# Optimization experiments

Hardware: AMD Instinct MI355X
Metric: run time of the kernel (lower is better)

## Reference

```python
import jax, jax.numpy as jnp
import numpy as np

B, N, C, L, E = 8, 8192, 256, 4, 131072  # graphs, nodes/graph, channels (in=hidden=out), layers, edges/graph


def setup_inputs() -> dict:
    key = jax.random.key(0)
    ks = jax.random.split(key, 9)
    batch_node_tsr = jax.random.normal(ks[0], (B, N, C), jnp.float32)
    edge_index = jax.random.randint(ks[1], (B, 2, E), 0, N, jnp.int32)
    batch_last_node_idx_list = jnp.arange(1, B + 1, dtype=jnp.int32) * N - 1
    s1 = 1.0 / np.sqrt(C)
    s2 = 1.0 / np.sqrt(2 * C)
    # Base GraphConv layers: out = x @ Wr.T + sum_nbr(x) @ Wn.T + b  (all CxC since in=hidden=out)
    base_Wr = jax.random.uniform(ks[2], (L, C, C), jnp.float32, -s1, s1)
    base_Wn = jax.random.uniform(ks[3], (L, C, C), jnp.float32, -s1, s1)
    base_b = jax.random.uniform(ks[4], (L, C), jnp.float32, -s1, s1)
    # Adapter GraphConv layers take concatenated (2C) input
    adapt_Wr = jax.random.uniform(ks[5], (L, C, 2 * C), jnp.float32, -s2, s2)
    adapt_Wn = jax.random.uniform(ks[6], (L, C, 2 * C), jnp.float32, -s2, s2)
    adapt_b = jax.random.uniform(ks[7], (L, C), jnp.float32, -s2, s2)
    return dict(batch_node_tsr=batch_node_tsr, base_Wr=base_Wr, base_Wn=base_Wn,
                base_b=base_b, adapt_Wr=adapt_Wr, adapt_Wn=adapt_Wn, adapt_b=adapt_b,
                edge_index=edge_index, batch_last_node_idx_list=batch_last_node_idx_list)


def reference(batch_node_tsr, base_Wr, base_Wn, base_b, adapt_Wr, adapt_Wn, adapt_b,
              edge_index, batch_last_node_idx_list):
    # Batch graphs PyG-style: offset per-graph node indices into one big graph
    offsets = (jnp.arange(B, dtype=edge_index.dtype) * N)[:, None]  # [B,1]
    src = (edge_index[:, 0, :] + offsets).reshape(-1)  # [B*E]
    dst = (edge_index[:, 1, :] + offsets).reshape(-1)  # [B*E]
    x = batch_node_tsr.reshape(B * N, C)

    def gconv(h, Wr, Wn, b):
        # GraphConv: root transform + sum-aggregated neighbor transform
        agg = jax.ops.segment_sum(h[src], dst, num_segments=B * N)
        return h @ Wr.T + agg @ Wn.T + b

    # Base encoder pass, keeping all latent embeds
    lat = [x]
    for i in range(L):
        lat.append(jax.nn.relu(gconv(lat[-1], base_Wr[i], base_Wn[i], base_b[i])))
    base_batch_embed = lat[-1].reshape(B, N, C)

    # Adapter pass: concat(base_latent[i+1], curr) -> adapter GraphConv -> relu
    curr = x
    for i in range(L):
        curr = jax.nn.relu(gconv(jnp.concatenate([lat[i + 1], curr], axis=-1),
                                 adapt_Wr[i], adapt_Wn[i], adapt_b[i]))
    adapter_batch_embed = curr.reshape(B, N, C)
    return base_batch_embed, adapter_batch_embed
```

## Files before the change

### kernel.cpp

```cpp
#include <hip/hip_runtime.h>

#define B_ 8
#define N_ 8192
#define C_ 256
#define L_ 4
#define E_ 131072
#define BN_ 65536
#define EDGES_ 1048576

typedef __attribute__((ext_vector_type(8))) short short8;
typedef __attribute__((ext_vector_type(4))) float f32x4;

__device__ __forceinline__ unsigned short f2bf(float f){
  unsigned int u = __builtin_bit_cast(unsigned int, f);
  u += 0x7fffu + ((u >> 16) & 1u);
  return (unsigned short)(u >> 16);
}
__device__ __forceinline__ float bf2f(unsigned short h){
  unsigned int u = ((unsigned int)h) << 16;
  return __builtin_bit_cast(float, u);
}

__launch_bounds__(256)
__global__ void cvt_bf16_k(const float* __restrict__ in, unsigned short* __restrict__ out, int n4){
  int t = blockIdx.x * 256 + threadIdx.x;
  if (t >= n4) return;
  float4 v = ((const float4*)in)[t];
  ushort4 o;
  o.x = f2bf(v.x); o.y = f2bf(v.y); o.z = f2bf(v.z); o.w = f2bf(v.w);
  ((ushort4*)out)[t] = o;
}

__launch_bounds__(256)
__global__ void hist_k(const int* __restrict__ ei, int* __restrict__ cnt){
  int t = blockIdx.x * 256 + threadIdx.x;
  int b = t >> 17, e = t & (E_ - 1);
  int dst = ei[b * (2 * E_) + E_ + e];
  atomicAdd(&cnt[(b << 13) + dst], 1);
}

__launch_bounds__(256)
__global__ void scan_k(const int* __restrict__ cnt, int* __restrict__ row_ptr, int* __restrict__ cursor){
  __shared__ int lsum[256];
  int t = threadIdx.x;
  int base = t << 8;
  int s = 0;
  for (int i = 0; i < 256; ++i) s += cnt[base + i];
  lsum[t] = s;
  __syncthreads();
  for (int d = 1; d < 256; d <<= 1){
    int v = (t >= d) ? lsum[t - d] : 0;
    __syncthreads();
    lsum[t] += v;
    __syncthreads();
  }
  int off = lsum[t] - s;
  for (int i = 0; i < 256; ++i){
    row_ptr[base + i] = off;
    cursor[base + i]  = off;
    off += cnt[base + i];
  }
  if (t == 255) row_ptr[BN_] = off;
}

__launch_bounds__(256)
__global__ void scat_k(const int* __restrict__ ei, int* __restrict__ cursor, int* __restrict__ col){
  int t = blockIdx.x * 256 + threadIdx.x;
  int b = t >> 17, e = t & (E_ - 1);
  int src = ei[b * (2 * E_) + e];
  int dst = ei[b * (2 * E_) + E_ + e];
  int pos = atomicAdd(&cursor[(b << 13) + dst], 1);
  col[pos] = (b << 13) + src;
}

__launch_bounds__(256)
__global__ void agg_k(const unsigned short* __restrict__ feat, const int* __restrict__ row_ptr,
                      const int* __restrict__ col, unsigned short* __restrict__ out){
  int w = threadIdx.x >> 6, lane = threadIdx.x & 63;
  int g = blockIdx.x & 7, sblk = blockIdx.x >> 3;
  int node = (g << 13) + (sblk << 2) + w;
  int beg = row_ptr[node], end = row_ptr[node + 1];
  int ch = lane << 2;
  float a0=0,a1=0,a2=0,a3=0,b0=0,b1=0,b2=0,b3=0;
  int e = beg;
  for (; e + 2 <= end; e += 2){
    int s0 = col[e], s1 = col[e + 1];
    ushort4 v0 = *(const ushort4*)(feat + ((size_t)s0 << 8) + ch);
    ushort4 v1 = *(const ushort4*)(feat + ((size_t)s1 << 8) + ch);
    a0 += bf2f(v0.x); a1 += bf2f(v0.y); a2 += bf2f(v0.z); a3 += bf2f(v0.w);
    b0 += bf2f(v1.x); b1 += bf2f(v1.y); b2 += bf2f(v1.z); b3 += bf2f(v1.w);
  }
  if (e < end){
    int s0 = col[e];
    ushort4 v0 = *(const ushort4*)(feat + ((size_t)s0 << 8) + ch);
    a0 += bf2f(v0.x); a1 += bf2f(v0.y); a2 += bf2f(v0.z); a3 += bf2f(v0.w);
  }
  ushort4 o;
  o.x = f2bf(a0 + b0); o.y = f2bf(a1 + b1); o.z = f2bf(a2 + b2); o.w = f2bf(a3 + b3);
  *(ushort4*)(out + ((size_t)node << 8) + ch) = o;
}

#define GLDS16(gp, lp) __builtin_amdgcn_global_load_lds( \
    (const __attribute__((address_space(1))) void*)(gp), \
    (__attribute__((address_space(3))) void*)(lp), 16, 0, 0)

template<int P>
__launch_bounds__(256)
__global__ void gemm_k(const unsigned short* __restrict__ A0, const unsigned short* __restrict__ A1,
                       const unsigned short* __restrict__ A2, const unsigned short* __restrict__ A3,
                       const unsigned short* __restrict__ W0, const unsigned short* __restrict__ W1,
                       const unsigned short* __restrict__ W2, const unsigned short* __restrict__ W3,
                       int ldw, const float* __restrict__ bias,
                       unsigned short* __restrict__ outb, float* __restrict__ outf){
  __shared__ unsigned short a_t[128 * 32];
  __shared__ unsigned short b_t[128 * 32];
  const unsigned short* As[4] = {A0, A1, A2, A3};
  const unsigned short* Ws[4] = {W0, W1, W2, W3};
  const int tn = blockIdx.x & 1, tm = blockIdx.x >> 1;
  const int m0 = tm << 7, n0 = tn << 7;
  const int t = threadIdx.x, lane = t & 63;
  const int w = t >> 6, wr = w >> 1, wc = w & 1;
  const int lrow = lane & 15, kg = lane >> 4;
  f32x4 acc[4][4] = {};
#pragma unroll
  for (int p = 0; p < P; ++p){
    const unsigned short* A = As[p] + (size_t)m0 * C_;
    const unsigned short* W = Ws[p] + (size_t)n0 * ldw;
    for (int k0 = 0; k0 < C_; k0 += 32){
#pragma unroll
      for (int c = t; c < 512; c += 256){
        int row = c >> 2, seg = c & 3;
        GLDS16(A + row * C_  + k0 + seg * 8, &a_t[c * 8]);
        GLDS16(W + row * ldw + k0 + seg * 8, &b_t[c * 8]);
      }
      __syncthreads();
      short8 af[4], bfr[4];
#pragma unroll
      for (int m = 0; m < 4; ++m)
        af[m] = *(const short8*)&a_t[((wr << 6) + (m << 4) + lrow) * 32 + (kg << 3)];
#pragma unroll
      for (int n = 0; n < 4; ++n)
        bfr[n] = *(const short8*)&b_t[((wc << 6) + (n << 4) + lrow) * 32 + (kg << 3)];
#pragma unroll
      for (int m = 0; m < 4; ++m)
#pragma unroll
        for (int n = 0; n < 4; ++n)
          acc[m][n] = __builtin_amdgcn_mfma_f32_16x16x32_bf16(af[m], bfr[n], acc[m][n], 0, 0, 0);
      __syncthreads();
    }
  }
#pragma unroll
  for (int n = 0; n < 4; ++n){
    int colg = n0 + (wc << 6) + (n << 4) + lrow;
    float bv = bias[colg];
#pragma unroll
    for (int m = 0; m < 4; ++m){
      int rbase = m0 + (wr << 6) + (m << 4) + (kg << 2);
#pragma unroll
      for (int j = 0; j < 4; ++j){
        float v = acc[m][n][j] + bv;
        v = v > 0.f ? v : 0.f;
        size_t idx = (size_t)(rbase + j) * C_ + colg;
        outb[idx] = f2bf(v);
        if (outf) outf[idx] = v;
      }
    }
  }
}

extern "C" void kernel_launch(void* const* d_in, const int* in_sizes, int n_in,
                              void* d_out, int out_size, void* d_ws, size_t ws_size,
                              hipStream_t stream){
  const float* x_f   = (const float*)d_in[0];
  const float* bWr_f = (const float*)d_in[1];
  const float* bWn_f = (const float*)d_in[2];
  const float* bB    = (const float*)d_in[3];
  const float* aWr_f = (const float*)d_in[4];
  const float* aWn_f = (const float*)d_in[5];
  const float* aB    = (const float*)d_in[6];
  const int*   ei    = (const int*)d_in[7];
  float* out = (float*)d_out;
  (void)in_sizes; (void)n_in; (void)out_size; (void)ws_size;

  char* p = (char*)d_ws;
  const size_t BUF = (size_t)BN_ * C_ * sizeof(unsigned short);
  auto alloc = [&](size_t bytes){ void* r = (void*)p; p += (bytes + 255) & ~(size_t)255; return r; };
  unsigned short* xb   = (unsigned short*)alloc(BUF);
  unsigned short* latA = (unsigned short*)alloc(BUF);
  unsigned short* latB = (unsigned short*)alloc(BUF);
  unsigned short* curA = (unsigned short*)alloc(BUF);
  unsigned short* curB = (unsigned short*)alloc(BUF);
  unsigned short* agg0 = (unsigned short*)alloc(BUF);
  unsigned short* agg1 = (unsigned short*)alloc(BUF);
  unsigned short* wbR  = (unsigned short*)alloc((size_t)L_ * C_ * C_ * 2);
  unsigned short* wbN  = (unsigned short*)alloc((size_t)L_ * C_ * C_ * 2);
  unsigned short* waR  = (unsigned short*)alloc((size_t)L_ * C_ * 2 * C_ * 2);
  unsigned short* waN  = (unsigned short*)alloc((size_t)L_ * C_ * 2 * C_ * 2);
  int* cnt     = (int*)alloc((size_t)BN_ * 4);
  int* row_ptr = (int*)alloc((size_t)(BN_ + 1) * 4);
  int* cursor  = (int*)alloc((size_t)BN_ * 4);
  int* colx    = (int*)alloc((size_t)EDGES_ * 4);

  cvt_bf16_k<<<BN_ * C_ / 4 / 256, 256, 0, stream>>>(x_f, xb, BN_ * C_ / 4);
  cvt_bf16_k<<<L_ * C_ * C_ / 4 / 256, 256, 0, stream>>>(bWr_f, wbR, L_ * C_ * C_ / 4);
  cvt_bf16_k<<<L_ * C_ * C_ / 4 / 256, 256, 0, stream>>>(bWn_f, wbN, L_ * C_ * C_ / 4);
  cvt_bf16_k<<<L_ * C_ * 2 * C_ / 4 / 256, 256, 0, stream>>>(aWr_f, waR, L_ * C_ * 2 * C_ / 4);
  cvt_bf16_k<<<L_ * C_ * 2 * C_ / 4 / 256, 256, 0, stream>>>(aWn_f, waN, L_ * C_ * 2 * C_ / 4);

  hipMemsetAsync(cnt, 0, (size_t)BN_ * 4, stream);
  hist_k<<<EDGES_ / 256, 256, 0, stream>>>(ei, cnt);
  scan_k<<<1, 256, 0, stream>>>(cnt, row_ptr, cursor);
  scat_k<<<EDGES_ / 256, 256, 0, stream>>>(ei, cursor, colx);

  const int AGG_GRID  = BN_ / 4;
  const int GEMM_GRID = (BN_ / 128) * (C_ / 128);

  const size_t WB = (size_t)C_ * C_;
  const size_t WA = (size_t)C_ * 2 * C_;

  agg_k<<<AGG_GRID, 256, 0, stream>>>(xb, row_ptr, colx, agg0);
  gemm_k<2><<<GEMM_GRID, 256, 0, stream>>>(xb, agg0, nullptr, nullptr,
      wbR, wbN, nullptr, nullptr, C_, bB, latA, nullptr);
  agg_k<<<AGG_GRID, 256, 0, stream>>>(latA, row_ptr, colx, agg1);
  gemm_k<2><<<GEMM_GRID, 256, 0, stream>>>(latA, agg1, nullptr, nullptr,
      wbR + WB, wbN + WB, nullptr, nullptr, C_, bB + 256, latB, nullptr);
  gemm_k<4><<<GEMM_GRID, 256, 0, stream>>>(latA, xb, agg1, agg0,
      waR, waR + 256, waN, waN + 256, 2 * C_, aB, curA, nullptr);
  agg_k<<<AGG_GRID, 256, 0, stream>>>(curA, row_ptr, colx, agg0);
  agg_k<<<AGG_GRID, 256, 0, stream>>>(latB, row_ptr, colx, agg1);
  gemm_k<2><<<GEMM_GRID, 256, 0, stream>>>(latB, agg1, nullptr, nullptr,
      wbR + 2 * WB, wbN + 2 * WB, nullptr, nullptr, C_, bB + 512, latA, nullptr);
  gemm_k<4><<<GEMM_GRID, 256, 0, stream>>>(latB, curA, agg1, agg0,
      waR + WA, waR + WA + 256, waN + WA, waN + WA + 256, 2 * C_, aB + 256, curB, nullptr);
  agg_k<<<AGG_GRID, 256, 0, stream>>>(curB, row_ptr, colx, agg0);
  agg_k<<<AGG_GRID, 256, 0, stream>>>(latA, row_ptr, colx, agg1);
  gemm_k<2><<<GEMM_GRID, 256, 0, stream>>>(latA, agg1, nullptr, nullptr,
      wbR + 3 * WB, wbN + 3 * WB, nullptr, nullptr, C_, bB + 768, latB, out);
  gemm_k<4><<<GEMM_GRID, 256, 0, stream>>>(latA, curB, agg1, agg0,
      waR + 2 * WA, waR + 2 * WA + 256, waN + 2 * WA, waN + 2 * WA + 256, 2 * C_, aB + 512, curA, nullptr);
  agg_k<<<AGG_GRID, 256, 0, stream>>>(curA, row_ptr, colx, agg0);
  agg_k<<<AGG_GRID, 256, 0, stream>>>(latB, row_ptr, colx, agg1);
  gemm_k<4><<<GEMM_GRID, 256, 0, stream>>>(latB, curA, agg1, agg0,
      waR + 3 * WA, waR + 3 * WA + 256, waN + 3 * WA, waN + 3 * WA + 256, 2 * C_, aB + 768,
      curB, out + (size_t)BN_ * C_);
}
```

Measured before the change: 1.240 ms.

## Fuse paired aggregations and widen GEMM tiles to full output width

Adds agg2_k, which gathers two feature tensors over the same CSR neighbour list in one pass, so index loads and launches are shared, and uses it in place of paired agg_k calls. The GEMM now gives each block 128 rows by all 256 output columns, so A tiles are loaded once instead of twice. Each wave computes 32x256, and bf16 output is staged through LDS for 16-byte coalesced stores. The last layer skips the unused bf16 store. The cost is more accumulator registers (128 floats per thread) and half as many GEMM blocks, which may reduce occupancy.

Result: no change. 1.248 ms (+0.7%).

```diff
diff --git a/kernel.cpp b/kernel.cpp
--- a/kernel.cpp
+++ b/kernel.cpp
@@ -100,6 +100,43 @@
   *(ushort4*)(out + ((size_t)node << 8) + ch) = o;
 }
 
+__launch_bounds__(256)
+__global__ void agg2_k(const unsigned short* __restrict__ fA, const unsigned short* __restrict__ fB,
+                       const int* __restrict__ row_ptr, const int* __restrict__ col,
+                       unsigned short* __restrict__ oA, unsigned short* __restrict__ oB){
+  int w = threadIdx.x >> 6, lane = threadIdx.x & 63;
+  int g = blockIdx.x & 7, sblk = blockIdx.x >> 3;
+  int node = (g << 13) + (sblk << 2) + w;
+  int beg = row_ptr[node], end = row_ptr[node + 1];
+  int ch = lane << 2;
+  float a0=0,a1=0,a2=0,a3=0, c0=0,c1=0,c2=0,c3=0;
+  float a4=0,a5=0,a6=0,a7=0, c4=0,c5=0,c6=0,c7=0;
+  int e = beg;
+  for (; e + 2 <= end; e += 2){
+    int s0 = col[e], s1 = col[e + 1];
+    ushort4 va0 = *(const ushort4*)(fA + ((size_t)s0 << 8) + ch);
+    ushort4 vb0 = *(const ushort4*)(fB + ((size_t)s0 << 8) + ch);
+    ushort4 va1 = *(const ushort4*)(fA + ((size_t)s1 << 8) + ch);
+    ushort4 vb1 = *(const ushort4*)(fB + ((size_t)s1 << 8) + ch);
+    a0 += bf2f(va0.x); a1 += bf2f(va0.y); a2 += bf2f(va0.z); a3 += bf2f(va0.w);
+    c0 += bf2f(vb0.x); c1 += bf2f(vb0.y); c2 += bf2f(vb0.z); c3 += bf2f(vb0.w);
+    a4 += bf2f(va1.x); a5 += bf2f(va1.y); a6 += bf2f(va1.z); a7 += bf2f(va1.w);
+    c4 += bf2f(vb1.x); c5 += bf2f(vb1.y); c6 += bf2f(vb1.z); c7 += bf2f(vb1.w);
+  }
+  if (e < end){
+    int s0 = col[e];
+    ushort4 va0 = *(const ushort4*)(fA + ((size_t)s0 << 8) + ch);
+    ushort4 vb0 = *(const ushort4*)(fB + ((size_t)s0 << 8) + ch);
+    a0 += bf2f(va0.x); a1 += bf2f(va0.y); a2 += bf2f(va0.z); a3 += bf2f(va0.w);
+    c0 += bf2f(vb0.x); c1 += bf2f(vb0.y); c2 += bf2f(vb0.z); c3 += bf2f(vb0.w);
+  }
+  ushort4 oa, ob;
+  oa.x = f2bf(a0 + a4); oa.y = f2bf(a1 + a5); oa.z = f2bf(a2 + a6); oa.w = f2bf(a3 + a7);
+  ob.x = f2bf(c0 + c4); ob.y = f2bf(c1 + c5); ob.z = f2bf(c2 + c6); ob.w = f2bf(c3 + c7);
+  *(ushort4*)(oA + ((size_t)node << 8) + ch) = oa;
+  *(ushort4*)(oB + ((size_t)node << 8) + ch) = ob;
+}
+
 #define GLDS16(gp, lp) __builtin_amdgcn_global_load_lds( \
     (const __attribute__((address_space(1))) void*)(gp), \
     (__attribute__((address_space(3))) void*)(lp), 16, 0, 0)
@@ -112,57 +149,88 @@
                        const unsigned short* __restrict__ W2, const unsigned short* __restrict__ W3,
                        int ldw, const float* __restrict__ bias,
                        unsigned short* __restrict__ outb, float* __restrict__ outf){
-  __shared__ unsigned short a_t[128 * 32];
-  __shared__ unsigned short b_t[128 * 32];
+  __shared__ unsigned short lds_u[12288];
+  unsigned short* a_t = lds_u;
+  unsigned short* b_t = lds_u + 4096;
   const unsigned short* As[4] = {A0, A1, A2, A3};
   const unsigned short* Ws[4] = {W0, W1, W2, W3};
-  const int tn = blockIdx.x & 1, tm = blockIdx.x >> 1;
-  const int m0 = tm << 7, n0 = tn << 7;
+  const int m0 = blockIdx.x << 7;
   const int t = threadIdx.x, lane = t & 63;
-  const int w = t >> 6, wr = w >> 1, wc = w & 1;
+  const int w = t >> 6;
   const int lrow = lane & 15, kg = lane >> 4;
-  f32x4 acc[4][4] = {};
+  f32x4 acc[2][16] = {};
 #pragma unroll
   for (int p = 0; p < P; ++p){
     const unsigned short* A = As[p] + (size_t)m0 * C_;
-    const unsigned short* W = Ws[p] + (size_t)n0 * ldw;
+    const unsigned short* W = Ws[p];
     for (int k0 = 0; k0 < C_; k0 += 32){
 #pragma unroll
       for (int c = t; c < 512; c += 256){
         int row = c >> 2, seg = c & 3;
         GLDS16(A + row * C_  + k0 + seg * 8, &a_t[c * 8]);
+      }
+#pragma unroll
+      for (int c = t; c < 1024; c += 256){
+        int row = c >> 2, seg = c & 3;
         GLDS16(W + row * ldw + k0 + seg * 8, &b_t[c * 8]);
       }
       __syncthreads();
-      short8 af[4], bfr[4];
-#pragma unroll
-      for (int m = 0; m < 4; ++m)
-        af[m] = *(const short8*)&a_t[((wr << 6) + (m << 4) + lrow) * 32 + (kg << 3)];
-#pragma unroll
-      for (int n = 0; n < 4; ++n)
-        bfr[n] = *(const short8*)&b_t[((wc << 6) + (n << 4) + lrow) * 32 + (kg << 3)];
-#pragma unroll
-      for (int m = 0; m < 4; ++m)
-#pragma unroll
-        for (int n = 0; n < 4; ++n)
-          acc[m][n] = __builtin_amdgcn_mfma_f32_16x16x32_bf16(af[m], bfr[n], acc[m][n], 0, 0, 0);
+      short8 af[2];
+#pragma unroll
+      for (int m = 0; m < 2; ++m)
+        af[m] = *(const short8*)&a_t[((w << 5) + (m << 4) + lrow) * 32 + (kg << 3)];
+#pragma unroll
+      for (int h = 0; h < 2; ++h){
+        short8 bfr[8];
+#pragma unroll
+        for (int n2 = 0; n2 < 8; ++n2)
+          bfr[n2] = *(const short8*)&b_t[((h << 7) + (n2 << 4) + lrow) * 32 + (kg << 3)];
+#pragma unroll
+        for (int m = 0; m < 2; ++m)
+#pragma unroll
+          for (int n2 = 0; n2 < 8; ++n2)
+            acc[m][(h << 3) + n2] =
+                __builtin_amdgcn_mfma_f32_16x16x32_bf16(af[m], bfr[n2], acc[m][(h << 3) + n2], 0, 0, 0);
+      }
       __syncthreads();
     }
   }
-#pragma unroll
-  for (int n = 0; n < 4; ++n){
-    int colg = n0 + (wc << 6) + (n << 4) + lrow;
-    float bv = bias[colg];
-#pragma unroll
-    for (int m = 0; m < 4; ++m){
-      int rbase = m0 + (wr << 6) + (m << 4) + (kg << 2);
-#pragma unroll
-      for (int j = 0; j < 4; ++j){
-        float v = acc[m][n][j] + bv;
-        v = v > 0.f ? v : 0.f;
-        size_t idx = (size_t)(rbase + j) * C_ + colg;
-        outb[idx] = f2bf(v);
-        if (outf) outf[idx] = v;
+  float bv[16];
+#pragma unroll
+  for (int n = 0; n < 16; ++n) bv[n] = bias[(n << 4) + lrow];
+  unsigned short* ep = lds_u + (w << 11);
+#pragma unroll
+  for (int m = 0; m < 2; ++m){
+    const int gr = m0 + (w << 5) + (m << 4);
+    if (outf){
+#pragma unroll
+      for (int n = 0; n < 16; ++n)
+#pragma unroll
+        for (int j = 0; j < 4; ++j){
+          float v = acc[m][n][j] + bv[n];
+          v = v > 0.f ? v : 0.f;
+          outf[(size_t)(gr + (kg << 2) + j) * C_ + (n << 4) + lrow] = v;
+        }
+    }
+    if (outb){
+#pragma unroll
+      for (int h = 0; h < 2; ++h){
+#pragma unroll
+        for (int n2 = 0; n2 < 8; ++n2){
+          int n = (h << 3) + n2;
+#pragma unroll
+          for (int j = 0; j < 4; ++j){
+            float v = acc[m][n][j] + bv[n];
+            v = v > 0.f ? v : 0.f;
+            ep[((kg << 2) + j) * 128 + (n2 << 4) + lrow] = f2bf(v);
+          }
+        }
+#pragma unroll
+        for (int k = 0; k < 4; ++k){
+          int r = (lane >> 4) + (k << 2);
+          short8 v = *(const short8*)&ep[r * 128 + (lane & 15) * 8];
+          *(short8*)&outb[(size_t)(gr + r) * C_ + (h << 7) + (lane & 15) * 8] = v;
+        }
       }
     }
   }
@@ -213,7 +281,7 @@
   scat_k<<<EDGES_ / 256, 256, 0, stream>>>(ei, cursor, colx);
 
   const int AGG_GRID  = BN_ / 4;
-  const int GEMM_GRID = (BN_ / 128) * (C_ / 128);
+  const int GEMM_GRID = BN_ / 128;
 
   const size_t WB = (size_t)C_ * C_;
   const size_t WA = (size_t)C_ * 2 * C_;
@@ -226,21 +294,18 @@
       wbR + WB, wbN + WB, nullptr, nullptr, C_, bB + 256, latB, nullptr);
   gemm_k<4><<<GEMM_GRID, 256, 0, stream>>>(latA, xb, agg1, agg0,
       waR, waR + 256, waN, waN + 256, 2 * C_, aB, curA, nullptr);
-  agg_k<<<AGG_GRID, 256, 0, stream>>>(curA, row_ptr, colx, agg0);
-  agg_k<<<AGG_GRID, 256, 0, stream>>>(latB, row_ptr, colx, agg1);
+  agg2_k<<<AGG_GRID, 256, 0, stream>>>(latB, curA, row_ptr, colx, agg1, agg0);
   gemm_k<2><<<GEMM_GRID, 256, 0, stream>>>(latB, agg1, nullptr, nullptr,
       wbR + 2 * WB, wbN + 2 * WB, nullptr, nullptr, C_, bB + 512, latA, nullptr);
   gemm_k<4><<<GEMM_GRID, 256, 0, stream>>>(latB, curA, agg1, agg0,
       waR + WA, waR + WA + 256, waN + WA, waN + WA + 256, 2 * C_, aB + 256, curB, nullptr);
-  agg_k<<<AGG_GRID, 256, 0, stream>>>(curB, row_ptr, colx, agg0);
-  agg_k<<<AGG_GRID, 256, 0, stream>>>(latA, row_ptr, colx, agg1);
+  agg2_k<<<AGG_GRID, 256, 0, stream>>>(latA, curB, row_ptr, colx, agg1, agg0);
   gemm_k<2><<<GEMM_GRID, 256, 0, stream>>>(latA, agg1, nullptr, nullptr,
       wbR + 3 * WB, wbN + 3 * WB, nullptr, nullptr, C_, bB + 768, latB, out);
   gemm_k<4><<<GEMM_GRID, 256, 0, stream>>>(latA, curB, agg1, agg0,
       waR + 2 * WA, waR + 2 * WA + 256, waN + 2 * WA, waN + 2 * WA + 256, 2 * C_, aB + 512, curA, nullptr);
-  agg_k<<<AGG_GRID, 256, 0, stream>>>(curA, row_ptr, colx, agg0);
-  agg_k<<<AGG_GRID, 256, 0, stream>>>(latB, row_ptr, colx, agg1);
+  agg2_k<<<AGG_GRID, 256, 0, stream>>>(latB, curA, row_ptr, colx, agg1, agg0);
   gemm_k<4><<<GEMM_GRID, 256, 0, stream>>>(latB, curA, agg1, agg0,
       waR + 3 * WA, waR + 3 * WA + 256, waN + 3 * WA, waN + 3 * WA + 256, 2 * C_, aB + 768,
-      curB, out + (size_t)BN_ * C_);
-}
+      nullptr, out + (size_t)BN_ * C_);
+}
```
